# Performance work log

Measured on AMD Instinct MI355X. Metric: run time of the kernel, lower is better.

## Reference

```python
import jax, jax.numpy as jnp
import numpy as np

L, N, IN = 512, 256, 6   # seq_len, batch, input_size(1)+5 PPs
H = 1024                 # hidden_size
NUM_LAYERS = 2


def _lstm_layer(x, h0, c0, Wih, Whh, bih, bhh):
    """x: (L, N, in_dim). PyTorch gate order: i, f, g, o."""
    b = bih + bhh  # (4H,)
    # precompute input projections for all timesteps: (L, N, 4H)
    x_proj = jnp.einsum('lni,gi->lng', x, Wih) + b

    def step(carry, xt):
        h, c = carry
        gates = xt + h @ Whh.T           # (N, 4H)
        i, f, g, o = jnp.split(gates, 4, axis=-1)
        i = jax.nn.sigmoid(i)
        f = jax.nn.sigmoid(f)
        g = jnp.tanh(g)
        o = jax.nn.sigmoid(o)
        c = f * c + i * g
        h = o * jnp.tanh(c)
        return (h, c), h

    (hT, cT), ys = jax.lax.scan(step, (h0, c0), x_proj)
    return ys, hT, cT


def setup_inputs() -> dict:
    key = jax.random.key(0)
    ks = jax.random.split(key, 16)
    s = 1.0 / np.sqrt(H)
    inp = {"sequence": jax.random.normal(ks[0], (L, N, IN), dtype=jnp.float32)}
    in_dims = [IN, H]
    for l in range(NUM_LAYERS):
        d = in_dims[l]
        inp[f"W_ih_{l}"] = jax.random.uniform(ks[1 + 4 * l], (4 * H, d), minval=-s, maxval=s, dtype=jnp.float32)
        inp[f"W_hh_{l}"] = jax.random.uniform(ks[2 + 4 * l], (4 * H, H), minval=-s, maxval=s, dtype=jnp.float32)
        inp[f"b_ih_{l}"] = jax.random.uniform(ks[3 + 4 * l], (4 * H,), minval=-s, maxval=s, dtype=jnp.float32)
        inp[f"b_hh_{l}"] = jax.random.uniform(ks[4 + 4 * l], (4 * H,), minval=-s, maxval=s, dtype=jnp.float32)
    inp["lin_W"] = jax.random.uniform(ks[9], (1, H), minval=-s, maxval=s, dtype=jnp.float32)
    inp["lin_b"] = jax.random.uniform(ks[10], (1,), minval=-s, maxval=s, dtype=jnp.float32)
    return inp


def reference(sequence, W_ih_0, W_hh_0, b_ih_0, b_hh_0,
              W_ih_1, W_hh_1, b_ih_1, b_hh_1, lin_W, lin_b):
    n = sequence.shape[1]
    h0 = jnp.zeros((n, H), dtype=sequence.dtype)
    c0 = jnp.zeros((n, H), dtype=sequence.dtype)
    params = [(W_ih_0, W_hh_0, b_ih_0, b_hh_0), (W_ih_1, W_hh_1, b_ih_1, b_hh_1)]
    x = sequence
    for (Wih, Whh, bih, bhh) in params:
        x, _, _ = _lstm_layer(x, h0, c0, Wih, Whh, bih, bhh)
    # linear on last timestep output -> (1, N, 1)
    out = (x[-1] @ lin_W.T + lin_b).reshape(1, n, 1)
    return out
```

## Files before the change

### kernel.cpp

```cpp
#include <hip/hip_runtime.h>
#include <cstdint>
#include <cstddef>

#define LSEQ 512
#define NBLK 256
#define ASZ (128*256*8)
#define NPLN 8

typedef _Float16 f16;
typedef f16 f16x8 __attribute__((ext_vector_type(8)));
typedef float f32x4 __attribute__((ext_vector_type(4)));
typedef unsigned long long u64t;
typedef unsigned int u32t;

#define MFMA16(a, b, c) __builtin_amdgcn_mfma_f32_16x16x32_f16(a, b, c, 0, 0, 0)

static __device__ __forceinline__ float sigm(float x){ return 1.f/(1.f+__expf(-x)); }
static __device__ __forceinline__ float tanh_f(float x){
    x = fminf(fmaxf(x,-15.f),15.f);
    float t = __expf(-2.f*x);
    return (1.f-t)/(1.f+t);
}

static __device__ __forceinline__ u64t hload(const u64t* p){
    return __hip_atomic_load(p, __ATOMIC_RELAXED, __HIP_MEMORY_SCOPE_AGENT);
}
static __device__ __forceinline__ void hstore(u64t* p, u64t v){
    __hip_atomic_store(p, v, __ATOMIC_RELAXED, __HIP_MEMORY_SCOPE_AGENT);
}
static __device__ __forceinline__ void hstore32(u32t* p, u32t v){
    __hip_atomic_store(p, v, __ATOMIC_RELAXED, __HIP_MEMORY_SCOPE_AGENT);
}
union U2F16x8 { u64t q[2]; f16x8 v; };

#define WAITVM0() __builtin_amdgcn_s_waitcnt(0x0F70)

static __device__ __forceinline__ void grid_barrier(int* bar, bool inv){
    WAITVM0();
    __syncthreads();
    if (threadIdx.x == 0){
        int g = __hip_atomic_load(&bar[32], __ATOMIC_RELAXED, __HIP_MEMORY_SCOPE_AGENT);
        int old = __hip_atomic_fetch_add(&bar[0], 1, __ATOMIC_RELAXED, __HIP_MEMORY_SCOPE_AGENT);
        if (old == NBLK - 1){
            __hip_atomic_store(&bar[0], 0, __ATOMIC_RELAXED, __HIP_MEMORY_SCOPE_AGENT);
            __hip_atomic_store(&bar[32], g + 1, __ATOMIC_RELAXED, __HIP_MEMORY_SCOPE_AGENT);
        } else {
            while (__hip_atomic_load(&bar[32], __ATOMIC_RELAXED, __HIP_MEMORY_SCOPE_AGENT) == g)
                __builtin_amdgcn_s_sleep(2);
        }
    }
    __syncthreads();
    if (inv) __builtin_amdgcn_fence(__ATOMIC_ACQUIRE, "agent");
}

__global__ void __launch_bounds__(256, 1) lstm_persist(
    const float* __restrict__ seq,
    const float* __restrict__ Wih0, const float* __restrict__ Whh0,
    const float* __restrict__ bih0, const float* __restrict__ bhh0,
    const float* __restrict__ Wih1, const float* __restrict__ Whh1,
    const float* __restrict__ bih1, const float* __restrict__ bhh1,
    const float* __restrict__ linW, const float* __restrict__ linb,
    f16* __restrict__ A0, f16* __restrict__ A1, f16* __restrict__ Wc,
    float* __restrict__ out, int* __restrict__ bar)
{
    __shared__ char  pool[34816] __attribute__((aligned(16)));
    __shared__ float ldsX[384];
    __shared__ float ldsWx[384];
    __shared__ float ldsB0[64];
    __shared__ float ldsB1[64];
    float* poolf = (float*)pool;

    const int tid = threadIdx.x, lane = tid & 63, wav = tid >> 6;
    const int quad = lane >> 4, l15 = lane & 15;
    const int nh = wav;
    const int blk = blockIdx.x, nb = blk & 63, mh = blk >> 6;
    const int m0 = mh * 64, j0 = nb * 16;

    if (tid < 64){
        int R = (tid >> 4) * 1024 + j0 + (tid & 15);
        ldsB0[tid] = bih0[R] + bhh0[R];
        ldsB1[tid] = bih1[R] + bhh1[R];
    }
    for (int t = tid; t < 384; t += 256){
        int ct = t / 6, i = t - ct * 6;
        int R = (ct >> 4) * 1024 + j0 + (ct & 15);
        ldsWx[t] = Wih0[(size_t)R * 6 + i];
    }

    if (blk < 64){
        const float* S[3] = {Whh0, Wih1, Whh1};
        #pragma unroll
        for (int mat = 0; mat < 3; ++mat){
            u32t* D = (u32t*)Wc + (size_t)mat * (2u << 20);
            const float* Sm = S[mat];
            for (int idx = tid; idx < 64 * 512; idx += 256){
                int ri = idx >> 9, pr = idx & 511;
                int R = (ri >> 4) * 1024 + j0 + (ri & 15);
                float2 f = *(const float2*)(Sm + (size_t)R * 1024 + pr * 2);
                union { f16 h[2]; u32t w; } pk;
                pk.h[0] = (f16)f.x; pk.h[1] = (f16)f.y;
                hstore32(D + (size_t)R * 512 + pr, pk.w);
            }
        }
    }
    grid_barrier(bar, true);

    const int Rw = nh * 1024 + j0 + l15;
    const char* pwBase = (const char*)Wc + ((size_t)Rw * 1024 + quad * 8) * 2;
    const char* pw0 = pwBase;
    const char* pw1 = pwBase + (8u << 20);
    const char* pw2 = pwBase + (16u << 20);
    const int Aoff = quad * 4096 + (m0 + l15) * 16;

    float cst[8];
    #pragma unroll
    for (int i = 0; i < 8; ++i) cst[i] = 0.f;

    for (int p = 0; p <= LSEQ; ++p){
        const char* P0 = (const char*)(A0 + (size_t)(p & 7) * ASZ);
        const char* P1 = (const char*)(A1 + (size_t)((p + 7) & 7) * ASZ);
        u64t* W0p = (u64t*)(A0 + (size_t)((p + 1) & 7) * ASZ);
        u64t* W1p = (u64t*)(A1 + (size_t)(p & 7) * ASZ);

        if (p < LSEQ)
            for (int i = tid; i < 384; i += 256)
                ldsX[i] = seq[(size_t)p * 1536 + m0 * 6 + i];

        f32x4 acc0[4], acc1[4];
        #pragma unroll
        for (int a = 0; a < 4; ++a){ acc0[a] = (f32x4){0,0,0,0}; acc1[a] = (f32x4){0,0,0,0}; }

        uint4 ab[4][4], wb[4][2];

#define LOADS(vc_, sl_) do{ \
        const char* Pa_ = ((vc_) < 32) ? P0 : P1; \
        const int cc_ = (vc_) & 31; \
        ab[sl_][0] = *(const uint4*)(Pa_ + (Aoff + cc_ * 16384 +   0)); \
        ab[sl_][1] = *(const uint4*)(Pa_ + (Aoff + cc_ * 16384 + 256)); \
        ab[sl_][2] = *(const uint4*)(Pa_ + (Aoff + cc_ * 16384 + 512)); \
        ab[sl_][3] = *(const uint4*)(Pa_ + (Aoff + cc_ * 16384 + 768)); \
        if ((vc_) < 32){ \
            wb[sl_][0] = *(const uint4*)(pw0 + cc_ * 64); \
            wb[sl_][1] = *(const uint4*)(pw1 + cc_ * 64); \
        } else { \
            wb[sl_][0] = *(const uint4*)(pw2 + cc_ * 64); \
        } }while(0)

        LOADS(0, 0); LOADS(1, 1); LOADS(2, 2);
        #pragma unroll
        for (int vc = 0; vc < 64; ++vc){
            if (vc < 61) LOADS(vc + 3, (vc + 3) & 3);
            {
                const int sl = vc & 3;
                if (vc < 32){
                    f16x8 b0 = __builtin_bit_cast(f16x8, wb[sl][0]);
                    f16x8 b1 = __builtin_bit_cast(f16x8, wb[sl][1]);
                    #pragma unroll
                    for (int mt = 0; mt < 4; ++mt){
                        f16x8 a = __builtin_bit_cast(f16x8, ab[sl][mt]);
                        acc0[mt] = MFMA16(a, b0, acc0[mt]);
                        acc1[mt] = MFMA16(a, b1, acc1[mt]);
                    }
                } else {
                    f16x8 b = __builtin_bit_cast(f16x8, wb[sl][0]);
                    #pragma unroll
                    for (int mt = 0; mt < 4; ++mt)
                        acc1[mt] = MFMA16(__builtin_bit_cast(f16x8, ab[sl][mt]), b, acc1[mt]);
                }
            }
            __builtin_amdgcn_sched_barrier(0);
        }
#undef LOADS

        __syncthreads();
        #pragma unroll
        for (int mt = 0; mt < 4; ++mt){
            int o = (nh * 16 + l15) * 68 + mt * 16 + quad * 4;
            *(f32x4*)(poolf + o)        = acc0[mt];
            *(f32x4*)(poolf + 4352 + o) = acc1[mt];
        }
        __syncthreads();
        if (tid < 128 && p < LSEQ){
            const int m_l = tid & 63, oct = tid >> 6;
            float xv[6];
            #pragma unroll
            for (int i = 0; i < 6; ++i) xv[i] = ldsX[m_l * 6 + i];
            f16 hh[8];
            #pragma unroll
            for (int s = 0; s < 8; ++s){
                int j = oct * 8 + s;
                float gv[4];
                #pragma unroll
                for (int g = 0; g < 4; ++g){
                    float v = poolf[(g * 16 + j) * 68 + m_l] + ldsB0[g * 16 + j];
                    #pragma unroll
                    for (int i = 0; i < 6; ++i) v += xv[i] * ldsWx[(g * 16 + j) * 6 + i];
                    gv[g] = v;
                }
                float I = sigm(gv[0]), F = sigm(gv[1]), G = tanh_f(gv[2]), O = sigm(gv[3]);
                float cn = F * cst[s] + I * G; cst[s] = cn;
                hh[s] = (f16)(O * tanh_f(cn));
            }
            const int kc8 = nb * 2 + oct;
            union { f16 h[8]; u64t q[2]; } pk;
            #pragma unroll
            for (int s = 0; s < 8; ++s) pk.h[s] = hh[s];
            u64t* dst = W0p + (size_t)(kc8 * 256 + m0 + m_l) * 2;
            hstore(dst,     pk.q[0]);
            hstore(dst + 1, pk.q[1]);
        } else if (tid >= 128 && p >= 1){
            const int t2 = tid - 128;
            const int m_l = t2 & 63, oct = t2 >> 6;
            f16 hh[8];
            #pragma unroll
            for (int s = 0; s < 8; ++s){
                int j = oct * 8 + s;
                float gv[4];
                #pragma unroll
                for (int g = 0; g < 4; ++g)
                    gv[g] = poolf[4352 + (g * 16 + j) * 68 + m_l] + ldsB1[g * 16 + j];
                float I = sigm(gv[0]), F = sigm(gv[1]), G = tanh_f(gv[2]), O = sigm(gv[3]);
                float cn = F * cst[s] + I * G; cst[s] = cn;
                hh[s] = (f16)(O * tanh_f(cn));
            }
            const int kc8 = nb * 2 + oct;
            union { f16 h[8]; u64t q[2]; } pk;
            #pragma unroll
            for (int s = 0; s < 8; ++s) pk.h[s] = hh[s];
            u64t* dst = W1p + (size_t)(kc8 * 256 + m0 + m_l) * 2;
            hstore(dst,     pk.q[0]);
            hstore(dst + 1, pk.q[1]);
        }
        grid_barrier(bar, (p & 3) == 3);
    }
    if (blk < 64){
        const u64t* hp = (const u64t*)A1;
        int n = blk * 4 + wav;
        float s = 0.f;
        #pragma unroll
        for (int u = 0; u < 2; ++u){
            int kc = u * 64 + lane;
            U2F16x8 t;
            t.q[0] = hload(hp + (size_t)(kc * 256 + n) * 2);
            t.q[1] = hload(hp + (size_t)(kc * 256 + n) * 2 + 1);
            #pragma unroll
            for (int j = 0; j < 8; ++j) s += (float)t.v[j] * linW[kc * 8 + j];
        }
        #pragma unroll
        for (int m = 32; m >= 1; m >>= 1) s += __shfl_xor(s, m, 64);
        if (lane == 0) out[n] = s + linb[0];
    }
}

static void* g_wbuf = nullptr;
static struct WBufInit {
    WBufInit(){
        void* p = nullptr;
        if (hipMalloc(&p, (size_t)24 << 20) == hipSuccess) g_wbuf = p;
    }
} g_wbuf_init;

extern "C" void kernel_launch(void* const* d_in, const int* in_sizes, int n_in,
                              void* d_out, int out_size, void* d_ws, size_t ws_size,
                              hipStream_t stream)
{
    (void)in_sizes; (void)n_in; (void)out_size; (void)ws_size;
    const float* seq  = (const float*)d_in[0];
    const float* Wih0 = (const float*)d_in[1];
    const float* Whh0 = (const float*)d_in[2];
    const float* bih0 = (const float*)d_in[3];
    const float* bhh0 = (const float*)d_in[4];
    const float* Wih1 = (const float*)d_in[5];
    const float* Whh1 = (const float*)d_in[6];
    const float* bih1 = (const float*)d_in[7];
    const float* bhh1 = (const float*)d_in[8];
    const float* linW = (const float*)d_in[9];
    const float* linb = (const float*)d_in[10];
    float* outp = (float*)d_out;

    char* ws = (char*)d_ws;
    f16* A0p = (f16*)ws;
    f16* A1p = (f16*)(ws + (4 << 20));
    int* bar = (int*)(ws + (16 << 20));
    f16* Wcp = g_wbuf ? (f16*)g_wbuf : (f16*)(ws + (17 << 20));

    (void)hipMemsetAsync(ws, 0, 1 << 19, stream);
    (void)hipMemsetAsync(ws + (4 << 20), 0, 1 << 19, stream);
    (void)hipMemsetAsync(bar, 0, 1024, stream);

    lstm_persist<<<dim3(NBLK), dim3(256), 0, stream>>>(
        seq, Wih0, Whh0, bih0, bhh0, Wih1, Whh1, bih1, bhh1, linW, linb,
        A0p, A1p, Wcp, outp, bar);
}
```

Before: 14.41 ms.

## Use hierarchical per-XCD grid barrier and XCD-aware block mapping

```diff
diff --git a/kernel.cpp b/kernel.cpp
--- a/kernel.cpp
+++ b/kernel.cpp
@@ -5,7 +5,7 @@
 #define LSEQ 512
 #define NBLK 256
 #define ASZ (128*256*8)
-#define NPLN 8
+#define NPLN 16
 
 typedef _Float16 f16;
 typedef f16 f16x8 __attribute__((ext_vector_type(8)));
@@ -35,17 +35,26 @@
 
 #define WAITVM0() __builtin_amdgcn_s_waitcnt(0x0F70)
 
-static __device__ __forceinline__ void grid_barrier(int* bar, bool inv){
+static __device__ __forceinline__ void grid_barrier(int* bar, int grp, bool inv){
     WAITVM0();
     __syncthreads();
     if (threadIdx.x == 0){
-        int g = __hip_atomic_load(&bar[32], __ATOMIC_RELAXED, __HIP_MEMORY_SCOPE_AGENT);
-        int old = __hip_atomic_fetch_add(&bar[0], 1, __ATOMIC_RELAXED, __HIP_MEMORY_SCOPE_AGENT);
-        if (old == NBLK - 1){
-            __hip_atomic_store(&bar[0], 0, __ATOMIC_RELAXED, __HIP_MEMORY_SCOPE_AGENT);
-            __hip_atomic_store(&bar[32], g + 1, __ATOMIC_RELAXED, __HIP_MEMORY_SCOPE_AGENT);
+        int g = __hip_atomic_load(&bar[160 + grp * 16], __ATOMIC_RELAXED, __HIP_MEMORY_SCOPE_AGENT);
+        int old = __hip_atomic_fetch_add(&bar[grp * 16], 1, __ATOMIC_RELAXED, __HIP_MEMORY_SCOPE_AGENT);
+        if (old == (NBLK / 8) - 1){
+            __hip_atomic_store(&bar[grp * 16], 0, __ATOMIC_RELAXED, __HIP_MEMORY_SCOPE_AGENT);
+            int r = __hip_atomic_fetch_add(&bar[128], 1, __ATOMIC_RELAXED, __HIP_MEMORY_SCOPE_AGENT);
+            if (r == 7){
+                __hip_atomic_store(&bar[128], 0, __ATOMIC_RELAXED, __HIP_MEMORY_SCOPE_AGENT);
+                #pragma unroll
+                for (int i = 0; i < 8; ++i)
+                    __hip_atomic_store(&bar[160 + i * 16], g + 1, __ATOMIC_RELAXED, __HIP_MEMORY_SCOPE_AGENT);
+            } else {
+                while (__hip_atomic_load(&bar[160 + grp * 16], __ATOMIC_RELAXED, __HIP_MEMORY_SCOPE_AGENT) == g)
+                    __builtin_amdgcn_s_sleep(1);
+            }
         } else {
-            while (__hip_atomic_load(&bar[32], __ATOMIC_RELAXED, __HIP_MEMORY_SCOPE_AGENT) == g)
+            while (__hip_atomic_load(&bar[160 + grp * 16], __ATOMIC_RELAXED, __HIP_MEMORY_SCOPE_AGENT) == g)
                 __builtin_amdgcn_s_sleep(2);
         }
     }
@@ -73,7 +82,9 @@
     const int tid = threadIdx.x, lane = tid & 63, wav = tid >> 6;
     const int quad = lane >> 4, l15 = lane & 15;
     const int nh = wav;
-    const int blk = blockIdx.x, nb = blk & 63, mh = blk >> 6;
+    const int blk = blockIdx.x;
+    const int xcd = blk & 7, kk = blk >> 3;
+    const int nb = xcd * 8 + (kk >> 2), mh = kk & 3;
     const int m0 = mh * 64, j0 = nb * 16;
 
     if (tid < 64){
@@ -87,15 +98,15 @@
         ldsWx[t] = Wih0[(size_t)R * 6 + i];
     }
 
-    if (blk < 64){
+    {
         const float* S[3] = {Whh0, Wih1, Whh1};
         #pragma unroll
         for (int mat = 0; mat < 3; ++mat){
             u32t* D = (u32t*)Wc + (size_t)mat * (2u << 20);
             const float* Sm = S[mat];
-            for (int idx = tid; idx < 64 * 512; idx += 256){
-                int ri = idx >> 9, pr = idx & 511;
-                int R = (ri >> 4) * 1024 + j0 + (ri & 15);
+            for (int idx = tid; idx < 16 * 512; idx += 256){
+                int r = idx >> 9, pr = idx & 511;
+                int R = blk * 16 + r;
                 float2 f = *(const float2*)(Sm + (size_t)R * 1024 + pr * 2);
                 union { f16 h[2]; u32t w; } pk;
                 pk.h[0] = (f16)f.x; pk.h[1] = (f16)f.y;
@@ -103,7 +114,7 @@
             }
         }
     }
-    grid_barrier(bar, true);
+    grid_barrier(bar, xcd, true);
 
     const int Rw = nh * 1024 + j0 + l15;
     const char* pwBase = (const char*)Wc + ((size_t)Rw * 1024 + quad * 8) * 2;
@@ -117,10 +128,10 @@
     for (int i = 0; i < 8; ++i) cst[i] = 0.f;
 
     for (int p = 0; p <= LSEQ; ++p){
-        const char* P0 = (const char*)(A0 + (size_t)(p & 7) * ASZ);
-        const char* P1 = (const char*)(A1 + (size_t)((p + 7) & 7) * ASZ);
-        u64t* W0p = (u64t*)(A0 + (size_t)((p + 1) & 7) * ASZ);
-        u64t* W1p = (u64t*)(A1 + (size_t)(p & 7) * ASZ);
+        const char* P0 = (const char*)(A0 + (size_t)(p & 15) * ASZ);
+        const char* P1 = (const char*)(A1 + (size_t)((p + 15) & 15) * ASZ);
+        u64t* W0p = (u64t*)(A0 + (size_t)((p + 1) & 15) * ASZ);
+        u64t* W1p = (u64t*)(A1 + (size_t)(p & 15) * ASZ);
 
         if (p < LSEQ)
             for (int i = tid; i < 384; i += 256)
@@ -231,7 +242,7 @@
             hstore(dst,     pk.q[0]);
             hstore(dst + 1, pk.q[1]);
         }
-        grid_barrier(bar, (p & 3) == 3);
+        grid_barrier(bar, xcd, (p & 7) == 7);
     }
     if (blk < 64){
         const u64t* hp = (const u64t*)A1;
@@ -280,13 +291,13 @@
 
     char* ws = (char*)d_ws;
     f16* A0p = (f16*)ws;
-    f16* A1p = (f16*)(ws + (4 << 20));
+    f16* A1p = (f16*)(ws + (8 << 20));
     int* bar = (int*)(ws + (16 << 20));
     f16* Wcp = g_wbuf ? (f16*)g_wbuf : (f16*)(ws + (17 << 20));
 
     (void)hipMemsetAsync(ws, 0, 1 << 19, stream);
-    (void)hipMemsetAsync(ws + (4 << 20), 0, 1 << 19, stream);
-    (void)hipMemsetAsync(bar, 0, 1024, stream);
+    (void)hipMemsetAsync(ws + (8 << 20), 0, 1 << 19, stream);
+    (void)hipMemsetAsync(bar, 0, 2048, stream);
 
     lstm_persist<<<dim3(NBLK), dim3(256), 0, stream>>>(
         seq, Wih0, Whh0, bih0, bhh0, Wih1, Whh1, bih1, bhh1, linW, linb,
```

Result: faster. 13.05 ms (-9.4%).
